# Optimization experiments

Measured on AMD Instinct MI355X. Metric: run time of the kernel, lower is better.

Reference implementation:

```python
import jax, jax.numpy as jnp
import numpy as np

B, S, E, D, V, H, NL = 16, 1024, 64, 256, 10000, 8, 3
HD = D // H


def _ln(x, g, b):
    m = jnp.mean(x, -1, keepdims=True)
    v = jnp.mean((x - m) ** 2, -1, keepdims=True)
    return (x - m) / jnp.sqrt(v + 1e-5) * g + b


def _mha(q_in, kv_in, in_w, in_b, out_w, out_b, causal):
    # torch nn.MultiheadAttention with packed in_proj [3D, D]
    d = q_in.shape[-1]
    q = q_in @ in_w[:d].T + in_b[:d]
    k = kv_in @ in_w[d:2 * d].T + in_b[d:2 * d]
    v = kv_in @ in_w[2 * d:].T + in_b[2 * d:]
    sp = lambda t: t.reshape(t.shape[0], t.shape[1], H, HD).transpose(0, 2, 1, 3)
    q, k, v = sp(q), sp(k), sp(v)
    s = jnp.einsum('bhqd,bhkd->bhqk', q, k) / jnp.float32(np.sqrt(HD))
    if causal:
        L = s.shape[-1]
        s = jnp.where(jnp.tril(jnp.ones((L, L), bool)), s, jnp.float32(-1e30))
    a = jax.nn.softmax(s, -1)
    o = jnp.einsum('bhqk,bhkd->bhqd', a, v).transpose(0, 2, 1, 3).reshape(q_in.shape[0], -1, d)
    return o @ out_w.T + out_b


def setup_inputs() -> dict:
    key = jax.random.key(0)
    ks = iter(jax.random.split(key, 40))
    n = lambda *sh: jax.random.normal(next(ks), sh, jnp.float32) * 0.05
    d = dict(
        tractovka=n(B, E), context=n(B, E), card=n(B, E),
        enc_w=n(3, D, E), enc_b=n(3, D),
        enc_ln_g=jnp.ones((3, D), jnp.float32), enc_ln_b=jnp.zeros((3, D), jnp.float32),
        fusion_w=n(D, 3 * D), fusion_b=n(D),
        fusion_ln_g=jnp.ones(D, jnp.float32), fusion_ln_b=jnp.zeros(D, jnp.float32),
        tok_emb=n(V, D), pos_emb=n(1024, D),
        sa_in_w=n(NL, 3 * D, D), sa_in_b=n(NL, 3 * D), sa_out_w=n(NL, D, D), sa_out_b=n(NL, D),
        ca_in_w=n(NL, 3 * D, D), ca_in_b=n(NL, 3 * D), ca_out_w=n(NL, D, D), ca_out_b=n(NL, D),
        ln1_g=jnp.ones((NL, D), jnp.float32), ln1_b=jnp.zeros((NL, D), jnp.float32),
        ln2_g=jnp.ones((NL, D), jnp.float32), ln2_b=jnp.zeros((NL, D), jnp.float32),
        ln3_g=jnp.ones((NL, D), jnp.float32), ln3_b=jnp.zeros((NL, D), jnp.float32),
        ffn_w1=n(NL, 4 * D, D), ffn_b1=n(NL, 4 * D), ffn_w2=n(NL, D, 4 * D), ffn_b2=n(NL, D),
        out_w=n(V, D), out_b=n(V),
        prev_tokens=jax.random.randint(next(ks), (B, S), 0, V, jnp.int32),
    )
    return d


def reference(tractovka, context, card, enc_w, enc_b, enc_ln_g, enc_ln_b,
              fusion_w, fusion_b, fusion_ln_g, fusion_ln_b, tok_emb, pos_emb,
              sa_in_w, sa_in_b, sa_out_w, sa_out_b, ca_in_w, ca_in_b, ca_out_w, ca_out_b,
              ln1_g, ln1_b, ln2_g, ln2_b, ln3_g, ln3_b,
              ffn_w1, ffn_b1, ffn_w2, ffn_b2, out_w, out_b, prev_tokens):
    enc = lambda x, i: jax.nn.gelu(_ln(x @ enc_w[i].T + enc_b[i], enc_ln_g[i], enc_ln_b[i]), approximate=False)
    mem = jnp.concatenate([enc(tractovka, 0), enc(context, 1), enc(card, 2)], -1)
    mem = jax.nn.gelu(_ln(mem @ fusion_w.T + fusion_b, fusion_ln_g, fusion_ln_b), approximate=False)[:, None, :]  # [B,1,D]
    x = tok_emb[prev_tokens] + pos_emb[:prev_tokens.shape[1]][None]  # [B,S,D]
    for i in range(NL):  # post-norm decoder layer: self-attn, cross-attn, ReLU FFN
        x = _ln(x + _mha(x, x, sa_in_w[i], sa_in_b[i], sa_out_w[i], sa_out_b[i], True), ln1_g[i], ln1_b[i])
        x = _ln(x + _mha(x, mem, ca_in_w[i], ca_in_b[i], ca_out_w[i], ca_out_b[i], False), ln2_g[i], ln2_b[i])
        x = _ln(x + (jax.nn.relu(x @ ffn_w1[i].T + ffn_b1[i]) @ ffn_w2[i].T + ffn_b2[i]), ln3_g[i], ln3_b[i])
    return x @ out_w.T + out_b  # [B,S,V]
```

## Files before the change

### kernel.cpp

```cpp
#include <hip/hip_runtime.h>
#include <math.h>

constexpr int B = 16, S = 1024, D = 256, E = 64, H = 8, HD = 32;

typedef __attribute__((ext_vector_type(8))) short bf16x8;
typedef __attribute__((ext_vector_type(4))) short bf16x4;
typedef __attribute__((ext_vector_type(4))) float f32x4;

__device__ __forceinline__ float gelu_f(float x) {
  return 0.5f * x * (1.0f + erff(x * 0.70710678118654752440f));
}

__device__ __forceinline__ unsigned short f2bf(float f) {
  union { float f; unsigned u; } x; x.f = f;
  unsigned r = x.u + 0x7fff + ((x.u >> 16) & 1);
  return (unsigned short)(r >> 16);
}

__device__ __forceinline__ unsigned cvt_pk_bf16(float a, float b) {
  unsigned r;
  asm("v_cvt_pk_bf16_f32 %0, %1, %2" : "=v"(r) : "v"(a), "v"(b));
  return r;
}

__device__ __forceinline__ void gl16(const void* g, void* l) {
  __builtin_amdgcn_global_load_lds(
      (const __attribute__((address_space(1))) void*)g,
      (__attribute__((address_space(3))) void*)l, 16, 0, 0);
}

__global__ void k_cvt_all(const float* __restrict__ s0, const float* __restrict__ s1,
                          const float* __restrict__ s2, const float* __restrict__ s3,
                          const float* __restrict__ s4, unsigned short* __restrict__ dst) {
  int i = (blockIdx.x * 256 + threadIdx.x) * 4;
  const float* src;
  int off;
  if (i < 589824)       { src = s0; off = i; }
  else if (i < 786432)  { src = s1; off = i - 589824; }
  else if (i < 1572864) { src = s2; off = i - 786432; }
  else if (i < 2359296) { src = s3; off = i - 1572864; }
  else                  { src = s4; off = i - 2359296; }
  float4 v = *(const float4*)(src + off);
  dst[i + 0] = f2bf(v.x);
  dst[i + 1] = f2bf(v.y);
  dst[i + 2] = f2bf(v.z);
  dst[i + 3] = f2bf(v.w);
}

__global__ void k_embed(const int* __restrict__ tok,
                        const float* __restrict__ tok_emb,
                        const float* __restrict__ pos_emb,
                        float* __restrict__ x, unsigned short* __restrict__ xb) {
  int t = threadIdx.x;
  int r = blockIdx.x * 4 + (t >> 6);
  int c4 = (t & 63) * 4;
  int s = r & (S - 1);
  int tk = tok[r];
  float4 te = *(const float4*)(tok_emb + (size_t)tk * D + c4);
  float4 pe = *(const float4*)(pos_emb + (size_t)s * D + c4);
  float4 v = make_float4(te.x + pe.x, te.y + pe.y, te.z + pe.z, te.w + pe.w);
  *(float4*)(x + (size_t)r * D + c4) = v;
  unsigned lo = cvt_pk_bf16(v.x, v.y), hi = cvt_pk_bf16(v.z, v.w);
  *(uint2*)(xb + (size_t)r * D + c4) = make_uint2(lo, hi);
}

__global__ __launch_bounds__(256)
void k_side(const float* __restrict__ tr, const float* __restrict__ ctx,
            const float* __restrict__ card,
            const float* __restrict__ enc_w, const float* __restrict__ enc_b,
            const float* __restrict__ eg, const float* __restrict__ ebt,
            const float* __restrict__ fw, const float* __restrict__ fb,
            const float* __restrict__ fg, const float* __restrict__ fbt,
            const float* __restrict__ ca_in_w, const float* __restrict__ ca_in_b,
            const float* __restrict__ ca_out_w, const float* __restrict__ ca_out_b,
            float* __restrict__ ca_add) {
  int b = blockIdx.x, d = threadIdx.x;
  __shared__ float catl[768], meml[256], vs[256];
  __shared__ float rw1[4], rw2[4];

  auto lnstat = [&](float acc, float& mean, float& rstd) {
    float a1 = acc, a2 = acc * acc;
#pragma unroll
    for (int off = 32; off > 0; off >>= 1) {
      a1 += __shfl_xor(a1, off);
      a2 += __shfl_xor(a2, off);
    }
    int wid = d >> 6, lane = d & 63;
    if (lane == 0) { rw1[wid] = a1; rw2[wid] = a2; }
    __syncthreads();
    float s1 = rw1[0] + rw1[1] + rw1[2] + rw1[3];
    float s2 = rw2[0] + rw2[1] + rw2[2] + rw2[3];
    mean = s1 * (1.0f / D);
    float var = s2 * (1.0f / D) - mean * mean;
    rstd = rsqrtf(var + 1e-5f);
    __syncthreads();
  };

  for (int i = 0; i < 3; ++i) {
    const float* xin = (i == 0 ? tr : (i == 1 ? ctx : card)) + b * E;
    const float* wr = enc_w + ((size_t)i * D + d) * E;
    float acc = enc_b[i * D + d];
#pragma unroll 8
    for (int e = 0; e < E; ++e) acc += xin[e] * wr[e];
    float mean, rstd;
    lnstat(acc, mean, rstd);
    float nv = (acc - mean) * rstd * eg[i * D + d] + ebt[i * D + d];
    catl[i * D + d] = gelu_f(nv);
  }
  __syncthreads();

  {
    const float* fwr = fw + (size_t)d * 768;
    float fa = fb[d];
    for (int k = 0; k < 768; ++k) fa += catl[k] * fwr[k];
    float mean, rstd;
    lnstat(fa, mean, rstd);
    meml[d] = gelu_f((fa - mean) * rstd * fg[d] + fbt[d]);
  }
  __syncthreads();

  for (int l = 0; l < 3; ++l) {
    const float* wi = ca_in_w + ((size_t)l * 768 + 512 + d) * 256;
    float v = ca_in_b[l * 768 + 512 + d];
    for (int k = 0; k < 256; ++k) v += meml[k] * wi[k];
    vs[d] = v;
    __syncthreads();
    const float* wo = ca_out_w + ((size_t)l * 256 + d) * 256;
    float o = ca_out_b[l * 256 + d];
    for (int k = 0; k < 256; ++k) o += vs[k] * wo[k];
    ca_add[((size_t)l * B + b) * 256 + d] = o;
    __syncthreads();
  }
}

__global__ __launch_bounds__(512)
void k_attn6(const unsigned short* __restrict__ qkv, unsigned short* __restrict__ out) {
  constexpr int KT = 64;
  __shared__ unsigned short Ks[2][KT * 32];
  __shared__ unsigned short Vt[2][32 * KT];
  __shared__ unsigned short Pl[8 * 32 * KT];

  const int t = threadIdx.x;
  const int w = t >> 6, lane = t & 63;
  const int lg = lane >> 4, lr = lane & 15;
  const int bh = blockIdx.y;
  const int h = bh & (H - 1), b = bh >> 3;
  const int qtile = (int)gridDim.x - 1 - (int)blockIdx.x;
  const int qb = qtile << 8;
  const int qw = qb + w * 32;
  const unsigned short* base = qkv + (size_t)b * S * 768 + h * HD;

  bf16x8 qf[2];
#pragma unroll
  for (int qr = 0; qr < 2; ++qr)
    qf[qr] = *(const bf16x8*)(base + (size_t)(qw + qr * 16 + lr) * 768 + lg * 8);

  f32x4 o[2][2];
#pragma unroll
  for (int qr = 0; qr < 2; ++qr)
#pragma unroll
    for (int dt = 0; dt < 2; ++dt) o[qr][dt] = (f32x4){0.f, 0.f, 0.f, 0.f};
  float mq[2], lq[2];
#pragma unroll
  for (int qr = 0; qr < 2; ++qr) { mq[qr] = -3.0e38f; lq[qr] = 0.f; }

  const float Cs = 0.17677669529663687f * 1.4426950408889634f;

  const int skey = t >> 2;
  const int sch = (t & 3) * 8;
  const int vkey = t >> 3;
  const int vch = (t & 7) * 4;
  char* pbase = (char*)Pl + (w << 12);

  const int nkt = (qb + 256) >> 6;

  if (t < 256) gl16(base + (size_t)skey * 768 + 256 + sch, (char*)Ks[0] + t * 16);
  bf16x4 vv = *(const bf16x4*)(base + (size_t)vkey * 768 + 512 + vch);
  __syncthreads();

  for (int kti = 0; kti < nkt; ++kti) {
    const int kt = kti << 6;
    const int cur = kti & 1;

#pragma unroll
    for (int j = 0; j < 4; ++j) {
      int d = vch + j;
      int byteo = d * (KT * 2) + ((vkey * 2) ^ ((d & 7) << 4));
      *(unsigned short*)((char*)Vt[cur] + byteo) = (unsigned short)vv[j];
    }
    if (kti + 1 < nkt) {
      if (t < 256)
        gl16(base + (size_t)(kt + KT + skey) * 768 + 256 + sch, (char*)Ks[cur ^ 1] + t * 16);
      vv = *(const bf16x4*)(base + (size_t)(kt + KT + vkey) * 768 + 512 + vch);
    }

    const bool active = (kt <= qw + 31);
    if (active) {
      bf16x8 kf[4];
#pragma unroll
      for (int t4 = 0; t4 < 4; ++t4)
        kf[t4] = *(const bf16x8*)&Ks[cur][(t4 * 16 + lr) * 32 + lg * 8];
      f32x4 sc[2][4];
      __builtin_amdgcn_s_setprio(1);
#pragma unroll
      for (int qr = 0; qr < 2; ++qr)
#pragma unroll
        for (int t4 = 0; t4 < 4; ++t4)
          sc[qr][t4] = __builtin_amdgcn_mfma_f32_16x16x32_bf16(
              kf[t4], qf[qr], (f32x4){0.f, 0.f, 0.f, 0.f}, 0, 0, 0);
      __builtin_amdgcn_s_setprio(0);

      if (kt + KT > qw) {
#pragma unroll
        for (int qr = 0; qr < 2; ++qr) {
          int q = qw + qr * 16 + lr;
#pragma unroll
          for (int t4 = 0; t4 < 4; ++t4)
#pragma unroll
            for (int r = 0; r < 4; ++r) {
              int k = kt + t4 * 16 + lg * 4 + r;
              if (k > q) sc[qr][t4][r] = -3.0e38f;
            }
        }
      }

#pragma unroll
      for (int qr = 0; qr < 2; ++qr) {
        float mx = sc[qr][0][0];
#pragma unroll
        for (int t4 = 0; t4 < 4; ++t4)
#pragma unroll
          for (int r = 0; r < 4; ++r) mx = fmaxf(mx, sc[qr][t4][r]);
        mx = fmaxf(mx, __shfl_xor(mx, 16));
        mx = fmaxf(mx, __shfl_xor(mx, 32));
        if (__any(mx > mq[qr] + 8.0f)) {
          float mn = fmaxf(mx, mq[qr]);
          float cf = exp2f((mq[qr] - mn) * Cs);
          mq[qr] = mn;
          lq[qr] *= cf;
#pragma unroll
          for (int r = 0; r < 4; ++r) {
            float cfo = __shfl(cf, (lane & 48) | (lg * 4 + r));
            o[qr][0][r] *= cfo;
            o[qr][1][r] *= cfo;
          }
        }
        float nmxC = -mq[qr] * Cs;
        float ps = 0.f;
#pragma unroll
        for (int t4 = 0; t4 < 4; ++t4)
#pragma unroll
          for (int r = 0; r < 4; ++r) {
            float p = exp2f(fmaf(sc[qr][t4][r], Cs, nmxC));
            sc[qr][t4][r] = p;
            ps += p;
          }
        lq[qr] += ps;
        int ql = qr * 16 + lr;
        int swz = (ql & 7) << 4;
        char* prow = pbase + ql * (KT * 2);
#pragma unroll
        for (int t4 = 0; t4 < 4; ++t4) {
          unsigned lo = cvt_pk_bf16(sc[qr][t4][0], sc[qr][t4][1]);
          unsigned hi = cvt_pk_bf16(sc[qr][t4][2], sc[qr][t4][3]);
          *(uint2*)(prow + ((t4 * 32 + lg * 8) ^ swz)) = make_uint2(lo, hi);
        }
      }
    }

    __syncthreads();

    if (active) {
#pragma unroll
      for (int kp = 0; kp < 2; ++kp) {
        bf16x8 vf[2], pf[2];
        int kb = kp * 64 + lg * 16;
#pragma unroll
        for (int dt = 0; dt < 2; ++dt) {
          int d = dt * 16 + lr;
          vf[dt] = *(const bf16x8*)((char*)Vt[cur] + d * (KT * 2) + (kb ^ ((d & 7) << 4)));
        }
#pragma unroll
        for (int qr = 0; qr < 2; ++qr) {
          int ql = qr * 16 + lr;
          pf[qr] = *(const bf16x8*)(pbase + ql * (KT * 2) + (kb ^ ((ql & 7) << 4)));
        }
        __builtin_amdgcn_s_setprio(1);
#pragma unroll
        for (int qr = 0; qr < 2; ++qr)
#pragma unroll
          for (int dt = 0; dt < 2; ++dt)
            o[qr][dt] = __builtin_amdgcn_mfma_f32_16x16x32_bf16(
                pf[qr], vf[dt], o[qr][dt], 0, 0, 0);
        __builtin_amdgcn_s_setprio(0);
      }
    }
  }

#pragma unroll
  for (int qr = 0; qr < 2; ++qr) {
    float ls = lq[qr];
    ls += __shfl_xor(ls, 16);
    ls += __shfl_xor(ls, 32);
    float invq = 1.0f / ls;
#pragma unroll
    for (int r = 0; r < 4; ++r) {
      float inv = __shfl(invq, (lane & 48) | (lg * 4 + r));
      int q = qw + qr * 16 + lg * 4 + r;
      unsigned short* orow = out + (size_t)(b * S + q) * D + h * HD;
#pragma unroll
      for (int dt = 0; dt < 2; ++dt)
        orow[dt * 16 + lr] = f2bf(o[qr][dt][r] * inv);
    }
  }
}

template <int EPI, int OUTBF, int SWZ>
__global__ __launch_bounds__(256)
void k_gemm_mfma(const unsigned short* __restrict__ A,
                 const unsigned short* __restrict__ W,
                 const float* __restrict__ bias,
                 void* __restrict__ Cout,
                 int M, int N, int K) {
  __shared__ unsigned short As[128][32];
  __shared__ unsigned short Bs[128][32];
  int t = threadIdx.x;
  int bx = blockIdx.x, by = blockIdx.y;
  if (SWZ) {
    int nx = gridDim.x;
    int lin = by * nx + bx;
    int q = (nx * (int)gridDim.y) >> 3;
    int nl = (lin & 7) * q + (lin >> 3);
    by = nl / nx;
    bx = nl - by * nx;
  }
  int row0 = by * 128, col0 = bx * 128;
  int wid = t >> 6, lane = t & 63;
  int wr = wid >> 1, wc = wid & 1;
  int lrow = lane & 15, lko = (lane >> 4) * 8;

  f32x4 acc[4][4];
#pragma unroll
  for (int mi = 0; mi < 4; ++mi)
#pragma unroll
    for (int ni = 0; ni < 4; ++ni)
      acc[mi][ni] = (f32x4){0.f, 0.f, 0.f, 0.f};

  int c0 = t, c1 = t + 256;
  int ar0 = c0 >> 2, aq0 = (c0 & 3) * 8;
  int ar1 = c1 >> 2, aq1 = (c1 & 3) * 8;
  int wrow0 = col0 + ar0; if (wrow0 > N - 1) wrow0 = N - 1;
  int wrow1 = col0 + ar1; if (wrow1 > N - 1) wrow1 = N - 1;

  const unsigned short* A0 = A + (size_t)(row0 + ar0) * K + aq0;
  const unsigned short* A1 = A + (size_t)(row0 + ar1) * K + aq1;
  const unsigned short* W0 = W + (size_t)wrow0 * K + aq0;
  const unsigned short* W1 = W + (size_t)wrow1 * K + aq1;

  for (int kt = 0; kt < K; kt += 32) {
    gl16(A0 + kt, (char*)As + c0 * 16);
    gl16(A1 + kt, (char*)As + c1 * 16);
    gl16(W0 + kt, (char*)Bs + c0 * 16);
    gl16(W1 + kt, (char*)Bs + c1 * 16);
    __syncthreads();

    bf16x8 af[4], bfr[4];
#pragma unroll
    for (int mi = 0; mi < 4; ++mi)
      af[mi] = *(const bf16x8*)&As[wr * 64 + mi * 16 + lrow][lko];
#pragma unroll
    for (int ni = 0; ni < 4; ++ni)
      bfr[ni] = *(const bf16x8*)&Bs[wc * 64 + ni * 16 + lrow][lko];
#pragma unroll
    for (int mi = 0; mi < 4; ++mi)
#pragma unroll
      for (int ni = 0; ni < 4; ++ni)
        acc[mi][ni] = __builtin_amdgcn_mfma_f32_16x16x32_bf16(af[mi], bfr[ni], acc[mi][ni], 0, 0, 0);
    __syncthreads();
  }

  int rbase = row0 + wr * 64 + (lane >> 4) * 4;
  int cbase = col0 + wc * 64 + lrow;
#pragma unroll
  for (int ni = 0; ni < 4; ++ni) {
    int c = cbase + ni * 16;
    if (c < N) {
      float bv = bias[c];
#pragma unroll
      for (int mi = 0; mi < 4; ++mi) {
        int rr = rbase + mi * 16;
#pragma unroll
        for (int r = 0; r < 4; ++r) {
          float v = acc[mi][ni][r] + bv;
          if (EPI == 1) v = fmaxf(v, 0.0f);
          size_t off = (size_t)(rr + r) * N + c;
          if (OUTBF)
            ((unsigned short*)Cout)[off] = f2bf(v);
          else
            ((float*)Cout)[off] = v;
        }
      }
    }
  }
}

template <int NLN>
__global__ __launch_bounds__(256)
void k_gemm_ln(const unsigned short* __restrict__ A,
               const unsigned short* __restrict__ W,
               const float* __restrict__ bias,
               const float* __restrict__ res,
               const float* __restrict__ ca,
               const float* __restrict__ g1, const float* __restrict__ b1,
               const float* __restrict__ g2, const float* __restrict__ b2,
               float* __restrict__ xout, unsigned short* __restrict__ xb,
               int K) {
  __shared__ unsigned short As[2][32][32];
  __shared__ unsigned short Bs[2][256][32];
  __shared__ float red[2][32][4];
  int t = threadIdx.x;
  int row0 = blockIdx.x * 32;
  int wc = t >> 6, lane = t & 63;
  int lr = lane & 15, lg = lane >> 4;

  f32x4 acc[2][4];
#pragma unroll
  for (int mi = 0; mi < 2; ++mi)
#pragma unroll
    for (int ni = 0; ni < 4; ++ni)
      acc[mi][ni] = (f32x4){0.f, 0.f, 0.f, 0.f};

  const unsigned short* srcA = nullptr;
  int adoff = 0;
  if (t < 128) {
    int rw = t >> 2, q = (t & 3) * 8;
    srcA = A + (size_t)(row0 + rw) * K + q;
    adoff = t * 16;
  }
  const unsigned short* srcB[4];
  int bdoff[4];
#pragma unroll
  for (int j = 0; j < 4; ++j) {
    int cb = t + (j << 8);
    int rw = cb >> 2, q = (cb & 3) * 8;
    srcB[j] = W + (size_t)rw * K + q;
    bdoff[j] = cb * 16;
  }

  const int nsteps = K >> 5;
  if (t < 128) gl16(srcA, (char*)As[0] + adoff);
#pragma unroll
  for (int j = 0; j < 4; ++j) gl16(srcB[j], (char*)Bs[0] + bdoff[j]);
  __syncthreads();

  for (int s = 0; s < nsteps; ++s) {
    const int cur = s & 1;
    if (s + 1 < nsteps) {
      int off = (s + 1) << 5;
      if (t < 128) gl16(srcA + off, (char*)As[cur ^ 1] + adoff);
#pragma unroll
      for (int j = 0; j < 4; ++j) gl16(srcB[j] + off, (char*)Bs[cur ^ 1] + bdoff[j]);
    }
    bf16x8 af[2], bfr[4];
#pragma unroll
    for (int mi = 0; mi < 2; ++mi)
      af[mi] = *(const bf16x8*)&As[cur][mi * 16 + lr][lg * 8];
#pragma unroll
    for (int ni = 0; ni < 4; ++ni)
      bfr[ni] = *(const bf16x8*)&Bs[cur][wc * 64 + ni * 16 + lr][lg * 8];
    __builtin_amdgcn_s_setprio(1);
#pragma unroll
    for (int mi = 0; mi < 2; ++mi)
#pragma unroll
      for (int ni = 0; ni < 4; ++ni)
        acc[mi][ni] = __builtin_amdgcn_mfma_f32_16x16x32_bf16(af[mi], bfr[ni], acc[mi][ni], 0, 0, 0);
    __builtin_amdgcn_s_setprio(0);
    __syncthreads();
  }

  int colb = wc * 64 + lr;
  float mean[2][4], rstd[2][4];

#pragma unroll
  for (int mi = 0; mi < 2; ++mi) {
#pragma unroll
    for (int r = 0; r < 4; ++r) {
      int rowl = mi * 16 + lg * 4 + r;
      int rowg = row0 + rowl;
      float s1 = 0.f, s2 = 0.f;
#pragma unroll
      for (int ni = 0; ni < 4; ++ni) {
        int c = colb + ni * 16;
        float v = acc[mi][ni][r] + bias[c] + res[(size_t)rowg * D + c];
        acc[mi][ni][r] = v;
        s1 += v; s2 += v * v;
      }
#pragma unroll
      for (int msk = 1; msk <= 8; msk <<= 1) {
        s1 += __shfl_xor(s1, msk);
        s2 += __shfl_xor(s2, msk);
      }
      if (lr == 0) { red[0][rowl][wc] = s1; red[1][rowl][wc] = s2; }
    }
  }
  __syncthreads();
#pragma unroll
  for (int mi = 0; mi < 2; ++mi)
#pragma unroll
    for (int r = 0; r < 4; ++r) {
      int rowl = mi * 16 + lg * 4 + r;
      f32x4 a = *(const f32x4*)&red[0][rowl][0];
      f32x4 bq = *(const f32x4*)&red[1][rowl][0];
      float s1 = a[0] + a[1] + a[2] + a[3];
      float s2 = bq[0] + bq[1] + bq[2] + bq[3];
      float mn = s1 * (1.0f / D);
      float vr = s2 * (1.0f / D) - mn * mn;
      mean[mi][r] = mn;
      rstd[mi][r] = rsqrtf(vr + 1e-5f);
    }
#pragma unroll
  for (int mi = 0; mi < 2; ++mi)
#pragma unroll
    for (int ni = 0; ni < 4; ++ni) {
      int c = colb + ni * 16;
      float gg = g1[c], bb = b1[c];
#pragma unroll
      for (int r = 0; r < 4; ++r)
        acc[mi][ni][r] = (acc[mi][ni][r] - mean[mi][r]) * rstd[mi][r] * gg + bb;
    }

  if (NLN == 2) {
    __syncthreads();
#pragma unroll
    for (int mi = 0; mi < 2; ++mi) {
#pragma unroll
      for (int r = 0; r < 4; ++r) {
        int rowl = mi * 16 + lg * 4 + r;
        int rowg = row0 + rowl;
        int bidx = rowg >> 10;
        float s1 = 0.f, s2 = 0.f;
#pragma unroll
        for (int ni = 0; ni < 4; ++ni) {
          int c = colb + ni * 16;
          float v = acc[mi][ni][r] + ca[(size_t)bidx * D + c];
          acc[mi][ni][r] = v;
          s1 += v; s2 += v * v;
        }
#pragma unroll
        for (int msk = 1; msk <= 8; msk <<= 1) {
          s1 += __shfl_xor(s1, msk);
          s2 += __shfl_xor(s2, msk);
        }
        if (lr == 0) { red[0][rowl][wc] = s1; red[1][rowl][wc] = s2; }
      }
    }
    __syncthreads();
#pragma unroll
    for (int mi = 0; mi < 2; ++mi)
#pragma unroll
      for (int r = 0; r < 4; ++r) {
        int rowl = mi * 16 + lg * 4 + r;
        f32x4 a = *(const f32x4*)&red[0][rowl][0];
        f32x4 bq = *(const f32x4*)&red[1][rowl][0];
        float s1 = a[0] + a[1] + a[2] + a[3];
        float s2 = bq[0] + bq[1] + bq[2] + bq[3];
        float mn = s1 * (1.0f / D);
        float vr = s2 * (1.0f / D) - mn * mn;
        mean[mi][r] = mn;
        rstd[mi][r] = rsqrtf(vr + 1e-5f);
      }
#pragma unroll
    for (int mi = 0; mi < 2; ++mi)
#pragma unroll
      for (int ni = 0; ni < 4; ++ni) {
        int c = colb + ni * 16;
        float gg = g2[c], bb = b2[c];
#pragma unroll
        for (int r = 0; r < 4; ++r)
          acc[mi][ni][r] = (acc[mi][ni][r] - mean[mi][r]) * rstd[mi][r] * gg + bb;
      }
  }

#pragma unroll
  for (int mi = 0; mi < 2; ++mi)
#pragma unroll
    for (int r = 0; r < 4; ++r) {
      int rowg = row0 + mi * 16 + lg * 4 + r;
#pragma unroll
      for (int ni = 0; ni < 4; ++ni) {
        int c = colb + ni * 16;
        float v = acc[mi][ni][r];
        xout[(size_t)rowg * D + c] = v;
        xb[(size_t)rowg * D + c] = f2bf(v);
      }
    }
}

extern "C" void kernel_launch(void* const* d_in, const int* in_sizes, int n_in,
                              void* d_out, int out_size, void* d_ws, size_t ws_size,
                              hipStream_t stream) {
  (void)in_sizes; (void)n_in; (void)out_size; (void)ws_size;
  const float* tractovka = (const float*)d_in[0];
  const float* context   = (const float*)d_in[1];
  const float* card      = (const float*)d_in[2];
  const float* enc_w     = (const float*)d_in[3];
  const float* enc_b     = (const float*)d_in[4];
  const float* enc_ln_g  = (const float*)d_in[5];
  const float* enc_ln_b  = (const float*)d_in[6];
  const float* fusion_w  = (const float*)d_in[7];
  const float* fusion_b  = (const float*)d_in[8];
  const float* fusion_ln_g = (const float*)d_in[9];
  const float* fusion_ln_b = (const float*)d_in[10];
  const float* tok_emb   = (const float*)d_in[11];
  const float* pos_emb   = (const float*)d_in[12];
  const float* sa_in_w   = (const float*)d_in[13];
  const float* sa_in_b   = (const float*)d_in[14];
  const float* sa_out_w  = (const float*)d_in[15];
  const float* sa_out_b  = (const float*)d_in[16];
  const float* ca_in_w   = (const float*)d_in[17];
  const float* ca_in_b   = (const float*)d_in[18];
  const float* ca_out_w  = (const float*)d_in[19];
  const float* ca_out_b  = (const float*)d_in[20];
  const float* ln1_g     = (const float*)d_in[21];
  const float* ln1_b     = (const float*)d_in[22];
  const float* ln2_g     = (const float*)d_in[23];
  const float* ln2_b     = (const float*)d_in[24];
  const float* ln3_g     = (const float*)d_in[25];
  const float* ln3_b     = (const float*)d_in[26];
  const float* ffn_w1    = (const float*)d_in[27];
  const float* ffn_b1    = (const float*)d_in[28];
  const float* ffn_w2    = (const float*)d_in[29];
  const float* ffn_b2    = (const float*)d_in[30];
  const float* out_w     = (const float*)d_in[31];
  const float* out_b     = (const float*)d_in[32];
  const int*   prev      = (const int*)d_in[33];
  float* out = (float*)d_out;

  const int M = B * S;

  float* ws = (float*)d_ws;
  float* x      = ws;
  float* bufA   = x + (size_t)M * D;
  float* bufB   = bufA + (size_t)M * 768;
  float* cat    = bufB + (size_t)M * D;
  float* mem    = cat + (size_t)B * 3 * D;
  float* ca_add = mem + (size_t)B * D;
  unsigned short* xb    = (unsigned short*)(ca_add + (size_t)3 * B * D);
  unsigned short* attnb = xb + (size_t)M * D;
  unsigned short* wbf   = attnb + (size_t)M * D;
  unsigned short* qkvb  = (unsigned short*)bufA;
  unsigned short* ffn1b = (unsigned short*)bufA;

  const int n_qkvw = 3 * 768 * D;
  const int n_outw = 3 * D * D;
  const int n_f1w  = 3 * 1024 * D;
  const int n_f2w  = 3 * D * 1024;
  unsigned short* w_qkv = wbf;
  unsigned short* w_out = w_qkv + n_qkvw;
  unsigned short* w_f1  = w_out + n_outw;
  unsigned short* w_f2  = w_f1 + n_f1w;
  unsigned short* w_v   = w_f2 + n_f2w;

  k_cvt_all<<<4804, 256, 0, stream>>>(sa_in_w, sa_out_w, ffn_w1, ffn_w2, out_w, wbf);

  k_embed<<<M / 4, 256, 0, stream>>>(prev, tok_emb, pos_emb, x, xb);
  k_side<<<B, 256, 0, stream>>>(tractovka, context, card,
                                enc_w, enc_b, enc_ln_g, enc_ln_b,
                                fusion_w, fusion_b, fusion_ln_g, fusion_ln_b,
                                ca_in_w, ca_in_b, ca_out_w, ca_out_b, ca_add);

  for (int l = 0; l < 3; ++l) {
    k_gemm_mfma<0, 1, 0><<<dim3(6, M / 128), 256, 0, stream>>>(
        xb, w_qkv + (size_t)l * 768 * D, sa_in_b + (size_t)l * 3 * D, qkvb,
        M, 768, D);
    k_attn6<<<dim3(S / 256, B * H), 512, 0, stream>>>(qkvb, attnb);
    k_gemm_ln<2><<<dim3(M / 32), 256, 0, stream>>>(
        attnb, w_out + (size_t)l * D * D, sa_out_b + (size_t)l * D,
        x, ca_add + (size_t)l * B * D,
        ln1_g + (size_t)l * D, ln1_b + (size_t)l * D,
        ln2_g + (size_t)l * D, ln2_b + (size_t)l * D,
        x, xb, D);
    k_gemm_mfma<1, 1, 0><<<dim3(8, M / 128), 256, 0, stream>>>(
        xb, w_f1 + (size_t)l * 1024 * D, ffn_b1 + (size_t)l * 4 * D, ffn1b,
        M, 1024, D);
    k_gemm_ln<1><<<dim3(M / 32), 256, 0, stream>>>(
        ffn1b, w_f2 + (size_t)l * D * 1024, ffn_b2 + (size_t)l * D,
        x, nullptr,
        ln3_g + (size_t)l * D, ln3_b + (size_t)l * D,
        nullptr, nullptr,
        x, xb, 1024);
  }
  k_gemm_mfma<0, 0, 1><<<dim3(79, M / 128), 256, 0, stream>>>(
      xb, w_v, out_b, out, M, 10000, D);
}
```

Measured before the change: 806.8 us.

## Skip fully masked key subtiles in causal attention; add 256x128 GEMM kernel

On the diagonal causal tile, the attention kernel now counts how many 16-key subtiles are still visible. It skips the QK MFMAs, the masking, the exp and half of the PV MFMAs for subtiles that are fully masked, saving wasted compute on diagonal blocks. Separately, a new 512-thread GEMM with a 256x128 tile replaces the 128x128 kernel for FFN1 and the vocab projection. This should give more A/W reuse per block at the cost of fewer blocks and more registers and LDS per block.

Result: no change. 805.4 us, median of 2 (-0.2%).

```diff
diff --git a/kernel.cpp b/kernel.cpp
--- a/kernel.cpp
+++ b/kernel.cpp
@@ -195,19 +195,24 @@
     }
 
     const bool active = (kt <= qw + 31);
+    int nvt4 = 4;
+    if (active && kt + KT > qw) nvt4 = ((qw + 31 - kt) >> 4) + 1;
+
     if (active) {
       bf16x8 kf[4];
 #pragma unroll
       for (int t4 = 0; t4 < 4; ++t4)
-        kf[t4] = *(const bf16x8*)&Ks[cur][(t4 * 16 + lr) * 32 + lg * 8];
+        if (t4 < nvt4)
+          kf[t4] = *(const bf16x8*)&Ks[cur][(t4 * 16 + lr) * 32 + lg * 8];
       f32x4 sc[2][4];
       __builtin_amdgcn_s_setprio(1);
 #pragma unroll
       for (int qr = 0; qr < 2; ++qr)
 #pragma unroll
         for (int t4 = 0; t4 < 4; ++t4)
-          sc[qr][t4] = __builtin_amdgcn_mfma_f32_16x16x32_bf16(
-              kf[t4], qf[qr], (f32x4){0.f, 0.f, 0.f, 0.f}, 0, 0, 0);
+          if (t4 < nvt4)
+            sc[qr][t4] = __builtin_amdgcn_mfma_f32_16x16x32_bf16(
+                kf[t4], qf[qr], (f32x4){0.f, 0.f, 0.f, 0.f}, 0, 0, 0);
       __builtin_amdgcn_s_setprio(0);
 
       if (kt + KT > qw) {
@@ -216,21 +221,25 @@
           int q = qw + qr * 16 + lr;
 #pragma unroll
           for (int t4 = 0; t4 < 4; ++t4)
-#pragma unroll
-            for (int r = 0; r < 4; ++r) {
-              int k = kt + t4 * 16 + lg * 4 + r;
-              if (k > q) sc[qr][t4][r] = -3.0e38f;
-            }
+            if (t4 < nvt4)
+#pragma unroll
+              for (int r = 0; r < 4; ++r) {
+                int k = kt + t4 * 16 + lg * 4 + r;
+                if (k > q) sc[qr][t4][r] = -3.0e38f;
+              }
         }
       }
 
 #pragma unroll
       for (int qr = 0; qr < 2; ++qr) {
-        float mx = sc[qr][0][0];
+        float mx = -3.0e38f;
 #pragma unroll
         for (int t4 = 0; t4 < 4; ++t4)
-#pragma unroll
-          for (int r = 0; r < 4; ++r) mx = fmaxf(mx, sc[qr][t4][r]);
+          if (t4 < nvt4) {
+            float a = fmaxf(fmaxf(sc[qr][t4][0], sc[qr][t4][1]),
+                            fmaxf(sc[qr][t4][2], sc[qr][t4][3]));
+            mx = fmaxf(mx, a);
+          }
         mx = fmaxf(mx, __shfl_xor(mx, 16));
         mx = fmaxf(mx, __shfl_xor(mx, 32));
         if (__any(mx > mq[qr] + 8.0f)) {
@@ -251,7 +260,7 @@
         for (int t4 = 0; t4 < 4; ++t4)
 #pragma unroll
           for (int r = 0; r < 4; ++r) {
-            float p = exp2f(fmaf(sc[qr][t4][r], Cs, nmxC));
+            float p = (t4 < nvt4) ? exp2f(fmaf(sc[qr][t4][r], Cs, nmxC)) : 0.0f;
             sc[qr][t4][r] = p;
             ps += p;
           }
@@ -273,6 +282,7 @@
     if (active) {
 #pragma unroll
       for (int kp = 0; kp < 2; ++kp) {
+        if (kp == 1 && nvt4 <= 2) break;
         bf16x8 vf[2], pf[2];
         int kb = kp * 64 + lg * 16;
 #pragma unroll
@@ -362,6 +372,93 @@
     gl16(A1 + kt, (char*)As + c1 * 16);
     gl16(W0 + kt, (char*)Bs + c0 * 16);
     gl16(W1 + kt, (char*)Bs + c1 * 16);
+    __syncthreads();
+
+    bf16x8 af[4], bfr[4];
+#pragma unroll
+    for (int mi = 0; mi < 4; ++mi)
+      af[mi] = *(const bf16x8*)&As[wr * 64 + mi * 16 + lrow][lko];
+#pragma unroll
+    for (int ni = 0; ni < 4; ++ni)
+      bfr[ni] = *(const bf16x8*)&Bs[wc * 64 + ni * 16 + lrow][lko];
+#pragma unroll
+    for (int mi = 0; mi < 4; ++mi)
+#pragma unroll
+      for (int ni = 0; ni < 4; ++ni)
+        acc[mi][ni] = __builtin_amdgcn_mfma_f32_16x16x32_bf16(af[mi], bfr[ni], acc[mi][ni], 0, 0, 0);
+    __syncthreads();
+  }
+
+  int rbase = row0 + wr * 64 + (lane >> 4) * 4;
+  int cbase = col0 + wc * 64 + lrow;
+#pragma unroll
+  for (int ni = 0; ni < 4; ++ni) {
+    int c = cbase + ni * 16;
+    if (c < N) {
+      float bv = bias[c];
+#pragma unroll
+      for (int mi = 0; mi < 4; ++mi) {
+        int rr = rbase + mi * 16;
+#pragma unroll
+        for (int r = 0; r < 4; ++r) {
+          float v = acc[mi][ni][r] + bv;
+          if (EPI == 1) v = fmaxf(v, 0.0f);
+          size_t off = (size_t)(rr + r) * N + c;
+          if (OUTBF)
+            ((unsigned short*)Cout)[off] = f2bf(v);
+          else
+            ((float*)Cout)[off] = v;
+        }
+      }
+    }
+  }
+}
+
+template <int EPI, int OUTBF, int SWZ>
+__global__ __launch_bounds__(512)
+void k_gemm_mfma2(const unsigned short* __restrict__ A,
+                  const unsigned short* __restrict__ W,
+                  const float* __restrict__ bias,
+                  void* __restrict__ Cout,
+                  int M, int N, int K) {
+  __shared__ unsigned short As[256][32];
+  __shared__ unsigned short Bs[128][32];
+  int t = threadIdx.x;
+  int bx = blockIdx.x, by = blockIdx.y;
+  if (SWZ) {
+    int nx = gridDim.x;
+    int lin = by * nx + bx;
+    int q = (nx * (int)gridDim.y) >> 3;
+    int nl = (lin & 7) * q + (lin >> 3);
+    by = nl / nx;
+    bx = nl - by * nx;
+  }
+  int row0 = by * 256, col0 = bx * 128;
+  int wid = t >> 6, lane = t & 63;
+  int wr = wid >> 1, wc = wid & 1;
+  int lrow = lane & 15, lko = (lane >> 4) * 8;
+
+  f32x4 acc[4][4];
+#pragma unroll
+  for (int mi = 0; mi < 4; ++mi)
+#pragma unroll
+    for (int ni = 0; ni < 4; ++ni)
+      acc[mi][ni] = (f32x4){0.f, 0.f, 0.f, 0.f};
+
+  int ca0 = t, ca1 = t + 512, cb = t;
+  int ar0 = ca0 >> 2, aq0 = (ca0 & 3) * 8;
+  int ar1 = ca1 >> 2, aq1 = (ca1 & 3) * 8;
+  int wrow = col0 + (cb >> 2); if (wrow > N - 1) wrow = N - 1;
+  int wq = (cb & 3) * 8;
+
+  const unsigned short* A0 = A + (size_t)(row0 + ar0) * K + aq0;
+  const unsigned short* A1 = A + (size_t)(row0 + ar1) * K + aq1;
+  const unsigned short* W0 = W + (size_t)wrow * K + wq;
+
+  for (int kt = 0; kt < K; kt += 32) {
+    gl16(A0 + kt, (char*)As + ca0 * 16);
+    gl16(A1 + kt, (char*)As + ca1 * 16);
+    gl16(W0 + kt, (char*)Bs + cb * 16);
     __syncthreads();
 
     bf16x8 af[4], bfr[4];
@@ -680,7 +777,7 @@
         ln1_g + (size_t)l * D, ln1_b + (size_t)l * D,
         ln2_g + (size_t)l * D, ln2_b + (size_t)l * D,
         x, xb, D);
-    k_gemm_mfma<1, 1, 0><<<dim3(8, M / 128), 256, 0, stream>>>(
+    k_gemm_mfma2<1, 1, 0><<<dim3(8, M / 256), 512, 0, stream>>>(
         xb, w_f1 + (size_t)l * 1024 * D, ffn_b1 + (size_t)l * 4 * D, ffn1b,
         M, 1024, D);
     k_gemm_ln<1><<<dim3(M / 32), 256, 0, stream>>>(
@@ -690,6 +787,6 @@
         nullptr, nullptr,
         x, xb, 1024);
   }
-  k_gemm_mfma<0, 0, 1><<<dim3(79, M / 128), 256, 0, stream>>>(
+  k_gemm_mfma2<0, 0, 1><<<dim3(79, M / 256), 512, 0, stream>>>(
       xb, w_v, out_b, out, M, 10000, D);
 }
```
